# Optimization experiments

Hardware: AMD Instinct MI355X
Metric: run time of the kernel (lower is better)

Reference implementation:

```python
import jax, jax.numpy as jnp
import numpy as np

N_NODES = 256  # num_eeg_channels; reshape in head forces node count == channels

def setup_inputs() -> dict:
    key = jax.random.key(0)
    ks = jax.random.split(key, 16)
    T, H, L, E = 30000, 512, 256, 32768
    def w(k, shape):
        return jax.random.normal(k, shape, jnp.float32) / np.sqrt(shape[0]).astype(np.float32)
    return {
        "eeg_nodes": jax.random.normal(ks[0], (N_NODES, T), jnp.float32),
        "eeg_idx": jax.random.randint(ks[1], (2, E), 0, N_NODES),
        "eeg_attr": jax.random.uniform(ks[2], (E,), jnp.float32),
        # struct_featurizer GIN: conv1 MLP [T,H,H], conv2 MLP [H,L,L]
        "Ws1a": w(ks[3], (T, H)), "bs1a": jnp.zeros((H,), jnp.float32),
        "Ws1b": w(ks[4], (H, H)), "bs1b": jnp.zeros((H,), jnp.float32),
        "Ws2a": w(ks[5], (H, L)), "bs2a": jnp.zeros((L,), jnp.float32),
        "Ws2b": w(ks[6], (L, L)), "bs2b": jnp.zeros((L,), jnp.float32),
        # gin_scorer GIN: conv1 MLP [L,H,H], conv2 MLP [H,1,1]
        "Wc1a": w(ks[7], (L, H)), "bc1a": jnp.zeros((H,), jnp.float32),
        "Wc1b": w(ks[8], (H, H)), "bc1b": jnp.zeros((H,), jnp.float32),
        "Wc2a": w(ks[9], (H, 1)), "bc2a": jnp.zeros((1,), jnp.float32),
        "Wc2b": w(ks[10], (1, 1)), "bc2b": jnp.zeros((1,), jnp.float32),
        # dementia head: Linear(N*L, 1)
        "Wd": w(ks[11], (N_NODES * L, 1)), "bd": jnp.zeros((1,), jnp.float32),
    }


def _gin_conv(x, src, dst, W1, b1, W2, b2):
    # GINConv, eps=0: nn(x + sum_{j in N(i)} x_j); edge weights unsupported/ignored.
    agg = jax.ops.segment_sum(x[src], dst, num_segments=N_NODES)
    h = x + agg
    h = jax.nn.relu(h @ W1 + b1)  # MLP([in, out, out]) = Linear-ReLU-Linear
    return h @ W2 + b2


def reference(eeg_nodes, eeg_idx, eeg_attr,
              Ws1a, bs1a, Ws1b, bs1b, Ws2a, bs2a, Ws2b, bs2b,
              Wc1a, bc1a, Wc1b, bc1b, Wc2a, bc2a, Wc2b, bc2b,
              Wd, bd):
    src, dst = eeg_idx[0], eeg_idx[1]
    # struct_featurizer (2-layer GIN; inter-layer ReLU, edge_weight ignored by GINConv)
    h = _gin_conv(eeg_nodes, src, dst, Ws1a, bs1a, Ws1b, bs1b)
    h = jax.nn.relu(h)
    feat = _gin_conv(h, src, dst, Ws2a, bs2a, Ws2b, bs2b)  # [N, L]
    # gin_scorer (2-layer GIN)
    s = _gin_conv(feat, src, dst, Wc1a, bc1a, Wc1b, bc1b)
    s = jax.nn.relu(s)
    s = _gin_conv(s, src, dst, Wc2a, bc2a, Wc2b, bc2b)  # [N, 1]
    region_scores = jax.nn.sigmoid(s)
    flat = feat.reshape(1, -1)  # [1, N*L]
    dementia_pred = jax.nn.sigmoid(flat @ Wd + bd)  # [1, 1]
    return dementia_pred, region_scores
```

## Files before the change

kernel.cpp:

```cpp
#include <hip/hip_runtime.h>
#include <math.h>

#define N_NODES 256
#define T_DIM   30000
#define KP      30016
#define H_DIM   512
#define L_DIM   256

typedef __attribute__((ext_vector_type(8))) short short8;
typedef __attribute__((ext_vector_type(4))) float floatx4;

__global__ void k_init_P(float* P, float* dem, float* u) {
    int t = blockIdx.x * blockDim.x + threadIdx.x;
    P[t] = ((t >> 8) == (t & 255)) ? 1.0f : 0.0f;
    if (t == 0) *dem = 0.0f;
    if (t < 256) u[t] = 0.0f;
}

__global__ void k_count_edges(const int* __restrict__ idx, int E, float* P) {
    int e = blockIdx.x * blockDim.x + threadIdx.x;
    if (e < E) {
        int s = idx[e];
        int d = idx[E + e];
        atomicAdd(&P[d * N_NODES + s], 1.0f);
    }
}

__global__ void k_zero(float* p, int n) {
    int t = blockIdx.x * blockDim.x + threadIdx.x;
    if (t < n) p[t] = 0.0f;
}

__device__ __forceinline__ unsigned short f2b(float f) {
    unsigned u = __float_as_uint(f);
    u += 0x7fffu + ((u >> 16) & 1u);
    return (unsigned short)(u >> 16);
}

__device__ __forceinline__ float4 zero4() {
    float4 z; z.x = z.y = z.z = z.w = 0.f; return z;
}

__global__ __launch_bounds__(256)
void k_wt(const float* __restrict__ W, unsigned short* __restrict__ Wt) {
    __shared__ float tile[64][65];
    const int k0 = blockIdx.x << 6;
    const int c0 = blockIdx.y << 6;
    const int t  = threadIdx.x;
    const int rr = t >> 4, c4 = (t & 15) << 2;
    #pragma unroll
    for (int i = 0; i < 4; ++i) {
        const int k = k0 + rr + (i << 4);
        float4 v = (k < T_DIM) ? *(const float4*)&W[(size_t)k * H_DIM + c0 + c4]
                               : zero4();
        tile[rr + (i << 4)][c4 + 0] = v.x;
        tile[rr + (i << 4)][c4 + 1] = v.y;
        tile[rr + (i << 4)][c4 + 2] = v.z;
        tile[rr + (i << 4)][c4 + 3] = v.w;
    }
    __syncthreads();
    const int cr = t >> 4, k4 = (t & 15) << 2;
    #pragma unroll
    for (int i = 0; i < 4; ++i) {
        const int c = cr + (i << 4);
        ushort4 o;
        o.x = f2b(tile[k4 + 0][c]);
        o.y = f2b(tile[k4 + 1][c]);
        o.z = f2b(tile[k4 + 2][c]);
        o.w = f2b(tile[k4 + 3][c]);
        *(ushort4*)&Wt[(size_t)(c0 + c) * KP + k0 + k4] = o;
    }
}

__global__ __launch_bounds__(256)
void k_gemm_bf16(const float* __restrict__ x, const unsigned short* __restrict__ Wt,
                 float* __restrict__ outp, int kc) {
    __shared__ __align__(16) unsigned short Al[128 * 64];
    __shared__ __align__(16) unsigned short Bl[128 * 64];

    const int t = threadIdx.x;
    const int orig = blockIdx.x;
    const int q = gridDim.x >> 3;
    const int L = (orig & 7) * q + (orig >> 3);
    const int tile = L & 7;
    const int colBase = (tile & 3) << 7;
    const int rowBase = (tile >> 2) << 7;
    const int z = L >> 3;
    const int kb0 = z * kc;
    const int kend = min(kb0 + kc, KP);
    const int nchunk = (kend - kb0) >> 6;

    const int ar  = t >> 4, afc = t & 15;
    const int br  = t >> 3, bhc = t & 7;
    const float*          axp = x  + (size_t)(rowBase + ar) * T_DIM + afc * 4;
    const unsigned short* bwp = Wt + (size_t)(colBase + br) * KP   + bhc * 8;

    const int w    = t >> 6;
    const int wr   = (w >> 1) << 6;
    const int wc   = (w & 1) << 6;
    const int lane = t & 63;
    const int lm   = lane & 15;
    const int lq   = (lane >> 4) << 3;

    floatx4 acc[4][4];
    #pragma unroll
    for (int i = 0; i < 4; ++i)
        #pragma unroll
        for (int j = 0; j < 4; ++j)
            acc[i][j] = (floatx4){0.f, 0.f, 0.f, 0.f};

    float4 pa[8];
    short8 pb[4];

#define GLOAD(C) do {                                                          \
        const int kg_ = kb0 + (C) * 64;                                        \
        const int ke_ = kg_ + afc * 4;                                         \
        _Pragma("unroll")                                                      \
        for (int i_ = 0; i_ < 8; ++i_)                                         \
            pa[i_] = (ke_ + 4 <= T_DIM)                                        \
                         ? *(const float4*)(axp + (size_t)(16 * i_) * T_DIM + kg_) \
                         : zero4();                                            \
        _Pragma("unroll")                                                      \
        for (int i_ = 0; i_ < 4; ++i_)                                         \
            pb[i_] = *(const short8*)(bwp + (size_t)(32 * i_) * KP + kg_);     \
    } while (0)

    GLOAD(0);

    #pragma unroll 1
    for (int c = 0; c < nchunk; ++c) {
        __syncthreads();
        #pragma unroll
        for (int i = 0; i < 8; ++i) {
            const int row = ar + 16 * i;
            const int ga  = (afc >> 1) ^ (row & 7);
            ushort4 uv;
            uv.x = f2b(pa[i].x); uv.y = f2b(pa[i].y);
            uv.z = f2b(pa[i].z); uv.w = f2b(pa[i].w);
            *(ushort4*)&Al[row * 64 + ga * 8 + (afc & 1) * 4] = uv;
        }
        #pragma unroll
        for (int i = 0; i < 4; ++i) {
            const int row = br + 32 * i;
            const int gb  = bhc ^ (row & 7);
            *(short8*)&Bl[row * 64 + gb * 8] = pb[i];
        }
        __syncthreads();

        if (c + 1 < nchunk) GLOAD(c + 1);

        #pragma unroll
        for (int s = 0; s < 2; ++s) {
            const int gbase = (s << 2) | (lq >> 3);
            short8 af[4], bf[4];
            #pragma unroll
            for (int i = 0; i < 4; ++i) {
                const int R = wr + i * 16 + lm;
                af[i] = *(const short8*)&Al[R * 64 + ((gbase ^ (R & 7)) << 3)];
            }
            #pragma unroll
            for (int j = 0; j < 4; ++j) {
                const int Cc = wc + j * 16 + lm;
                bf[j] = *(const short8*)&Bl[Cc * 64 + ((gbase ^ (Cc & 7)) << 3)];
            }
            #pragma unroll
            for (int i = 0; i < 4; ++i)
                #pragma unroll
                for (int j = 0; j < 4; ++j)
                    acc[i][j] = __builtin_amdgcn_mfma_f32_16x16x32_bf16(
                        af[i], bf[j], acc[i][j], 0, 0, 0);
        }
    }
#undef GLOAD

    float* op = outp + (size_t)z * (N_NODES * H_DIM);
    const int rq = (lane >> 4) << 2;
    #pragma unroll
    for (int i = 0; i < 4; ++i) {
        #pragma unroll
        for (int j = 0; j < 4; ++j) {
            const int r  = rowBase + wr + i * 16 + rq;
            const int cc = colBase + wc + j * 16 + lm;
            op[(size_t)(r + 0) * H_DIM + cc] = acc[i][j][0];
            op[(size_t)(r + 1) * H_DIM + cc] = acc[i][j][1];
            op[(size_t)(r + 2) * H_DIM + cc] = acc[i][j][2];
            op[(size_t)(r + 3) * H_DIM + cc] = acc[i][j][3];
        }
    }
}

__global__ __launch_bounds__(256)
void k_gemm_big_atomic(const float* __restrict__ x, const float* __restrict__ W,
                       float* __restrict__ outp, int kc) {
    __shared__ float xs[16 * 140];
    __shared__ float ws[16 * 132];
    const int t  = threadIdx.x;
    const int colBase = blockIdx.x * 128;
    const int rowBase = blockIdx.y * 128;
    const int kb0  = blockIdx.z * kc;
    const int kend = min(kb0 + kc, T_DIM);
    const int nchunk = (kend > kb0) ? ((kend - kb0) >> 4) : 0;
    const int lr  = t >> 2, lkq = (t & 3) * 4;
    const int wkk = t >> 5, wcq = (t & 31) * 4;
    const int tx  = t & 15, ty = t >> 4;
    float acc[8][8];
    #pragma unroll
    for (int i = 0; i < 8; ++i)
        #pragma unroll
        for (int j = 0; j < 8; ++j) acc[i][j] = 0.0f;
    #pragma unroll 1
    for (int c = 0; c < nchunk; ++c) {
        int kb = kb0 + c * 16;
        __syncthreads();
        const float* xp = x + (size_t)(rowBase + lr) * T_DIM + kb + lkq;
        float4 xa = *(const float4*)xp;
        float4 xb = *(const float4*)(xp + (size_t)64 * T_DIM);
        const float* wp = W + (size_t)(kb + wkk) * H_DIM + colBase + wcq;
        float4 wa = *(const float4*)wp;
        float4 wb = *(const float4*)(wp + 8 * H_DIM);
        xs[(lkq + 0) * 140 + lr] = xa.x; xs[(lkq + 1) * 140 + lr] = xa.y;
        xs[(lkq + 2) * 140 + lr] = xa.z; xs[(lkq + 3) * 140 + lr] = xa.w;
        xs[(lkq + 0) * 140 + lr + 64] = xb.x; xs[(lkq + 1) * 140 + lr + 64] = xb.y;
        xs[(lkq + 2) * 140 + lr + 64] = xb.z; xs[(lkq + 3) * 140 + lr + 64] = xb.w;
        *(float4*)&ws[wkk * 132 + wcq]       = wa;
        *(float4*)&ws[(wkk + 8) * 132 + wcq] = wb;
        __syncthreads();
        #pragma unroll
        for (int kk = 0; kk < 16; ++kk) {
            float a[8], b[8];
            *(float4*)&a[0] = *(const float4*)&xs[kk * 140 + ty * 8];
            *(float4*)&a[4] = *(const float4*)&xs[kk * 140 + ty * 8 + 4];
            *(float4*)&b[0] = *(const float4*)&ws[kk * 132 + tx * 8];
            *(float4*)&b[4] = *(const float4*)&ws[kk * 132 + tx * 8 + 4];
            #pragma unroll
            for (int i = 0; i < 8; ++i)
                #pragma unroll
                for (int j = 0; j < 8; ++j)
                    acc[i][j] = fmaf(a[i], b[j], acc[i][j]);
        }
    }
    if (nchunk == 0) return;
    #pragma unroll
    for (int i = 0; i < 8; ++i) {
        int r = rowBase + ty * 8 + i;
        #pragma unroll
        for (int j = 0; j < 8; ++j)
            atomicAdd(&outp[r * H_DIM + colBase + tx * 8 + j], acc[i][j]);
    }
}

__global__ void k_reduce(const float2* __restrict__ Y1p, float2* __restrict__ Y1,
                         int nz) {
    int i = blockIdx.x * blockDim.x + threadIdx.x;
    float2 s = Y1p[i];
    for (int z = 1; z < nz; ++z) {
        float2 v = Y1p[(size_t)z * 65536 + i];
        s.x += v.x; s.y += v.y;
    }
    Y1[i] = s;
}

template<int K, int N, int MODE>
__global__ __launch_bounds__(256)
void k_mstage(const float* __restrict__ A, const float* __restrict__ B,
              const float* __restrict__ bias, float* __restrict__ out, int act,
              const float* __restrict__ Wd, float* __restrict__ dem,
              const float* __restrict__ uW, float* __restrict__ u) {
    const int t = threadIdx.x;
    const int wv = (blockIdx.x << 2) | (t >> 6);
    const int nct = N >> 4;
    const int r0 = (wv / nct) << 4;
    const int c0 = (wv % nct) << 4;
    const int lane = t & 63;
    const int lm   = lane & 15;
    const int lq   = (lane >> 4) << 3;

    floatx4 accE = {0.f, 0.f, 0.f, 0.f};
    floatx4 accO = {0.f, 0.f, 0.f, 0.f};
    const float* ap = A + (size_t)(r0 + lm) * K + lq;
    const float* bp = B + (size_t)lq * N + c0 + lm;

    #pragma unroll 2
    for (int kb = 0; kb < K; kb += 64) {
        {
            float4 a0 = *(const float4*)(ap + kb);
            float4 a1 = *(const float4*)(ap + kb + 4);
            const float* bq = bp + (size_t)kb * N;
            float b0 = bq[0],           b1 = bq[(size_t)N];
            float b2 = bq[(size_t)2*N], b3 = bq[(size_t)3*N];
            float b4 = bq[(size_t)4*N], b5 = bq[(size_t)5*N];
            float b6 = bq[(size_t)6*N], b7 = bq[(size_t)7*N];
            short8 af, bf;
            af[0] = (short)f2b(a0.x); af[1] = (short)f2b(a0.y);
            af[2] = (short)f2b(a0.z); af[3] = (short)f2b(a0.w);
            af[4] = (short)f2b(a1.x); af[5] = (short)f2b(a1.y);
            af[6] = (short)f2b(a1.z); af[7] = (short)f2b(a1.w);
            bf[0] = (short)f2b(b0); bf[1] = (short)f2b(b1);
            bf[2] = (short)f2b(b2); bf[3] = (short)f2b(b3);
            bf[4] = (short)f2b(b4); bf[5] = (short)f2b(b5);
            bf[6] = (short)f2b(b6); bf[7] = (short)f2b(b7);
            accE = __builtin_amdgcn_mfma_f32_16x16x32_bf16(af, bf, accE, 0, 0, 0);
        }
        {
            const int k2 = kb + 32;
            float4 a0 = *(const float4*)(ap + k2);
            float4 a1 = *(const float4*)(ap + k2 + 4);
            const float* bq = bp + (size_t)k2 * N;
            float b0 = bq[0],           b1 = bq[(size_t)N];
            float b2 = bq[(size_t)2*N], b3 = bq[(size_t)3*N];
            float b4 = bq[(size_t)4*N], b5 = bq[(size_t)5*N];
            float b6 = bq[(size_t)6*N], b7 = bq[(size_t)7*N];
            short8 af, bf;
            af[0] = (short)f2b(a0.x); af[1] = (short)f2b(a0.y);
            af[2] = (short)f2b(a0.z); af[3] = (short)f2b(a0.w);
            af[4] = (short)f2b(a1.x); af[5] = (short)f2b(a1.y);
            af[6] = (short)f2b(a1.z); af[7] = (short)f2b(a1.w);
            bf[0] = (short)f2b(b0); bf[1] = (short)f2b(b1);
            bf[2] = (short)f2b(b2); bf[3] = (short)f2b(b3);
            bf[4] = (short)f2b(b4); bf[5] = (short)f2b(b5);
            bf[6] = (short)f2b(b6); bf[7] = (short)f2b(b7);
            accO = __builtin_amdgcn_mfma_f32_16x16x32_bf16(af, bf, accO, 0, 0, 0);
        }
    }

    const float bb = bias ? bias[c0 + lm] : 0.f;
    const int rq = (lane >> 4) << 2;
    float v[4];
    #pragma unroll
    for (int i = 0; i < 4; ++i) {
        v[i] = accE[i] + accO[i] + bb;
        if (act) v[i] = fmaxf(v[i], 0.f);
    }

    if (MODE == 2) {
        const float uw = uW[c0 + lm];
        #pragma unroll
        for (int i = 0; i < 4; ++i) {
            float p = v[i] * uw;
            #pragma unroll
            for (int off = 8; off; off >>= 1) p += __shfl_down(p, off, 16);
            if (lm == 0) atomicAdd(&u[r0 + rq + i], p);
        }
        return;
    }
    #pragma unroll
    for (int i = 0; i < 4; ++i)
        out[(size_t)(r0 + rq + i) * N + c0 + lm] = v[i];
    if (MODE == 1) {
        float p = 0.f;
        #pragma unroll
        for (int i = 0; i < 4; ++i)
            p += v[i] * Wd[(r0 + rq + i) * 256 + c0 + lm];
        #pragma unroll
        for (int off = 32; off; off >>= 1) p += __shfl_down(p, off, 64);
        if (lane == 0) atomicAdd(dem, p);
    }
}

__device__ __forceinline__ float sigmoidf(float x) {
    return 1.0f / (1.0f + expf(-x));
}

__global__ __launch_bounds__(256)
void k_final(const float* __restrict__ P, const float* __restrict__ u,
             const float* __restrict__ dem,
             const float* __restrict__ bc2a, const float* __restrict__ Wc2b,
             const float* __restrict__ bc2b, const float* __restrict__ bd,
             float* __restrict__ out) {
    __shared__ float red[4];
    const int b = blockIdx.x, t = threadIdx.x;
    float pv = P[b * 256 + t] * u[t];
    #pragma unroll
    for (int off = 32; off; off >>= 1) pv += __shfl_down(pv, off, 64);
    if ((t & 63) == 0) red[t >> 6] = pv;
    __syncthreads();
    if (t == 0) {
        float v = red[0] + red[1] + red[2] + red[3];
        float h2 = fmaxf(v + bc2a[0], 0.f);
        out[1 + b] = sigmoidf(h2 * Wc2b[0] + bc2b[0]);
        if (b == 0) out[0] = sigmoidf(*dem + bd[0]);
    }
}

extern "C" void kernel_launch(void* const* d_in, const int* in_sizes, int n_in,
                              void* d_out, int out_size, void* d_ws, size_t ws_size,
                              hipStream_t stream) {
    const float* x    = (const float*)d_in[0];
    const int*   idx  = (const int*)d_in[1];
    const float* Ws1a = (const float*)d_in[3];
    const float* bs1a = (const float*)d_in[4];
    const float* Ws1b = (const float*)d_in[5];
    const float* bs1b = (const float*)d_in[6];
    const float* Ws2a = (const float*)d_in[7];
    const float* bs2a = (const float*)d_in[8];
    const float* Ws2b = (const float*)d_in[9];
    const float* bs2b = (const float*)d_in[10];
    const float* Wc1a = (const float*)d_in[11];
    const float* bc1a = (const float*)d_in[12];
    const float* Wc1b = (const float*)d_in[13];
    const float* bc1b = (const float*)d_in[14];
    const float* Wc2a = (const float*)d_in[15];
    const float* bc2a = (const float*)d_in[16];
    const float* Wc2b = (const float*)d_in[17];
    const float* bc2b = (const float*)d_in[18];
    const float* Wd   = (const float*)d_in[19];
    const float* bd   = (const float*)d_in[20];
    float* out = (float*)d_out;
    const int E = in_sizes[1] / 2;

    float* w    = (float*)d_ws;
    float* P    = w;
    float* Y1   = P + 65536;
    float* bufA = Y1 + 131072;
    float* bufB = bufA + 131072;
    float* feat = bufB + 131072;
    float* u    = feat + 65536;
    float* dem  = u + 256;
    float* WtF  = dem + 64;
    const size_t WT_F = ((size_t)H_DIM * KP) / 2;
    float* Y1p  = WtF + WT_F;
    unsigned short* Wt = (unsigned short*)WtF;

    const long long fixed = (long long)(Y1p - w);
    const long long avail = (long long)(ws_size / 4) - fixed;
    int maxsplit = (avail > 0) ? (int)(avail / 131072) : 0;
    int nz = 0, kc = 0;
    const int CH64 = 469;
    if (maxsplit >= 2) {
        int splits = maxsplit < 56 ? maxsplit : 56;
        int cps = (CH64 + splits - 1) / splits;
        nz = (CH64 + cps - 1) / cps;
        kc = cps * 64;
    }

    k_init_P<<<256, 256, 0, stream>>>(P, dem, u);
    k_count_edges<<<(E + 255) / 256, 256, 0, stream>>>(idx, E, P);

    if (nz > 0) {
        k_wt<<<dim3(469, 8), 256, 0, stream>>>(Ws1a, Wt);
        k_gemm_bf16<<<8 * nz, 256, 0, stream>>>(x, Wt, Y1p, kc);
        k_reduce<<<256, 256, 0, stream>>>((const float2*)Y1p, (float2*)Y1, nz);
    } else {
        k_zero<<<512, 256, 0, stream>>>(Y1, N_NODES * H_DIM);
        k_gemm_big_atomic<<<dim3(4, 2, 63), 256, 0, stream>>>(x, Ws1a, Y1, 480);
    }

    k_mstage<256, 512, 0><<<128, 256, 0, stream>>>(P,    Y1,   bs1a, bufA, 1, 0, 0, 0, 0);
    k_mstage<512, 512, 0><<<128, 256, 0, stream>>>(bufA, Ws1b, bs1b, bufB, 1, 0, 0, 0, 0);
    k_mstage<256, 512, 0><<<128, 256, 0, stream>>>(P,    bufB, 0,    bufA, 0, 0, 0, 0, 0);
    k_mstage<512, 256, 0><<< 64, 256, 0, stream>>>(bufA, Ws2a, bs2a, bufB, 1, 0, 0, 0, 0);
    k_mstage<256, 256, 1><<< 64, 256, 0, stream>>>(bufB, Ws2b, bs2b, feat, 0, Wd, dem, 0, 0);
    k_mstage<256, 256, 0><<< 64, 256, 0, stream>>>(P,    feat, 0,    bufA, 0, 0, 0, 0, 0);
    k_mstage<256, 512, 0><<<128, 256, 0, stream>>>(bufA, Wc1a, bc1a, bufB, 1, 0, 0, 0, 0);
    k_mstage<512, 512, 2><<<128, 256, 0, stream>>>(bufB, Wc1b, bc1b, 0,    1, 0, 0, Wc2a, u);
    k_final<<<256, 256, 0, stream>>>(P, u, dem, bc2a, Wc2b, bc2b, bd, out);
}
```

Baseline: 260.8 us.

## Pre-convert x to bf16 in a fused prep kernel and reshape small-GEMM launches

A single k_prep launch now does the W transpose to bf16, converts x to a padded bf16 copy, and initialises P, dem and u. Folding these into one kernel cuts launch count, and the big GEMM then loads bf16 activations directly instead of converting fp32 on each tile. The max split-K count rises from 56 to 96, and the reduce kernel uses float4 accesses. The k_mstage kernels switch to one wave per block with 4x more blocks, which spreads work over more CUs. The cost is an extra full pass writing x as bf16 plus more partial sums for the reduce to sum.

```diff
diff --git a/kernel.cpp b/kernel.cpp
--- a/kernel.cpp
+++ b/kernel.cpp
@@ -10,11 +10,78 @@
 typedef __attribute__((ext_vector_type(8))) short short8;
 typedef __attribute__((ext_vector_type(4))) float floatx4;
 
-__global__ void k_init_P(float* P, float* dem, float* u) {
-    int t = blockIdx.x * blockDim.x + threadIdx.x;
-    P[t] = ((t >> 8) == (t & 255)) ? 1.0f : 0.0f;
-    if (t == 0) *dem = 0.0f;
-    if (t < 256) u[t] = 0.0f;
+__device__ __forceinline__ unsigned short f2b(float f) {
+    unsigned u = __float_as_uint(f);
+    u += 0x7fffu + ((u >> 16) & 1u);
+    return (unsigned short)(u >> 16);
+}
+
+__device__ __forceinline__ float4 zero4() {
+    float4 z; z.x = z.y = z.z = z.w = 0.f; return z;
+}
+
+__global__ __launch_bounds__(256)
+void k_prep(const float* __restrict__ W, const float* __restrict__ x,
+            unsigned short* __restrict__ Wt, unsigned short* __restrict__ xb,
+            float* __restrict__ P, float* __restrict__ dem,
+            float* __restrict__ u) {
+    __shared__ float tile[64][65];
+    const int b = blockIdx.x, t = threadIdx.x;
+    if (b < 3752) {
+        const int k0 = (b % 469) << 6;
+        const int c0 = (b / 469) << 6;
+        const int rr = t >> 4, c4 = (t & 15) << 2;
+        #pragma unroll
+        for (int i = 0; i < 4; ++i) {
+            const int k = k0 + rr + (i << 4);
+            float4 v = (k < T_DIM)
+                           ? *(const float4*)&W[(size_t)k * H_DIM + c0 + c4]
+                           : zero4();
+            tile[rr + (i << 4)][c4 + 0] = v.x;
+            tile[rr + (i << 4)][c4 + 1] = v.y;
+            tile[rr + (i << 4)][c4 + 2] = v.z;
+            tile[rr + (i << 4)][c4 + 3] = v.w;
+        }
+        __syncthreads();
+        const int cr = t >> 4, k4 = (t & 15) << 2;
+        #pragma unroll
+        for (int i = 0; i < 4; ++i) {
+            const int c = cr + (i << 4);
+            ushort4 o;
+            o.x = f2b(tile[k4 + 0][c]);
+            o.y = f2b(tile[k4 + 1][c]);
+            o.z = f2b(tile[k4 + 2][c]);
+            o.w = f2b(tile[k4 + 3][c]);
+            *(ushort4*)&Wt[(size_t)(c0 + c) * KP + k0 + k4] = o;
+        }
+    } else if (b < 7504) {
+        const int e0 = (b - 3752) * 2048 + t * 8;
+        const int row = e0 / KP;
+        const int col = e0 % KP;
+        short8 o;
+        if (col < T_DIM) {
+            float4 v0 = *(const float4*)&x[(size_t)row * T_DIM + col];
+            float4 v1 = *(const float4*)&x[(size_t)row * T_DIM + col + 4];
+            o[0] = (short)f2b(v0.x); o[1] = (short)f2b(v0.y);
+            o[2] = (short)f2b(v0.z); o[3] = (short)f2b(v0.w);
+            o[4] = (short)f2b(v1.x); o[5] = (short)f2b(v1.y);
+            o[6] = (short)f2b(v1.z); o[7] = (short)f2b(v1.w);
+        } else {
+            o = (short8){0, 0, 0, 0, 0, 0, 0, 0};
+        }
+        *(short8*)&xb[e0] = o;
+    } else if (b < 7568) {
+        const int i0 = ((b - 7504) << 10) + (t << 2);
+        float4 v;
+        v.x = ((i0 + 0) >> 8) == ((i0 + 0) & 255) ? 1.f : 0.f;
+        v.y = ((i0 + 1) >> 8) == ((i0 + 1) & 255) ? 1.f : 0.f;
+        v.z = ((i0 + 2) >> 8) == ((i0 + 2) & 255) ? 1.f : 0.f;
+        v.w = ((i0 + 3) >> 8) == ((i0 + 3) & 255) ? 1.f : 0.f;
+        *(float4*)&P[i0] = v;
+    } else {
+        if (t < 256) u[t] = 0.f;
+        if (t == 0) *dem = 0.f;
+    }
 }
 
 __global__ void k_count_edges(const int* __restrict__ idx, int E, float* P) {
@@ -26,54 +93,21 @@
     }
 }
 
+__global__ void k_init_P(float* P, float* dem, float* u) {
+    int t = blockIdx.x * blockDim.x + threadIdx.x;
+    P[t] = ((t >> 8) == (t & 255)) ? 1.0f : 0.0f;
+    if (t == 0) *dem = 0.0f;
+    if (t < 256) u[t] = 0.0f;
+}
+
 __global__ void k_zero(float* p, int n) {
     int t = blockIdx.x * blockDim.x + threadIdx.x;
     if (t < n) p[t] = 0.0f;
 }
 
-__device__ __forceinline__ unsigned short f2b(float f) {
-    unsigned u = __float_as_uint(f);
-    u += 0x7fffu + ((u >> 16) & 1u);
-    return (unsigned short)(u >> 16);
-}
-
-__device__ __forceinline__ float4 zero4() {
-    float4 z; z.x = z.y = z.z = z.w = 0.f; return z;
-}
-
 __global__ __launch_bounds__(256)
-void k_wt(const float* __restrict__ W, unsigned short* __restrict__ Wt) {
-    __shared__ float tile[64][65];
-    const int k0 = blockIdx.x << 6;
-    const int c0 = blockIdx.y << 6;
-    const int t  = threadIdx.x;
-    const int rr = t >> 4, c4 = (t & 15) << 2;
-    #pragma unroll
-    for (int i = 0; i < 4; ++i) {
-        const int k = k0 + rr + (i << 4);
-        float4 v = (k < T_DIM) ? *(const float4*)&W[(size_t)k * H_DIM + c0 + c4]
-                               : zero4();
-        tile[rr + (i << 4)][c4 + 0] = v.x;
-        tile[rr + (i << 4)][c4 + 1] = v.y;
-        tile[rr + (i << 4)][c4 + 2] = v.z;
-        tile[rr + (i << 4)][c4 + 3] = v.w;
-    }
-    __syncthreads();
-    const int cr = t >> 4, k4 = (t & 15) << 2;
-    #pragma unroll
-    for (int i = 0; i < 4; ++i) {
-        const int c = cr + (i << 4);
-        ushort4 o;
-        o.x = f2b(tile[k4 + 0][c]);
-        o.y = f2b(tile[k4 + 1][c]);
-        o.z = f2b(tile[k4 + 2][c]);
-        o.w = f2b(tile[k4 + 3][c]);
-        *(ushort4*)&Wt[(size_t)(c0 + c) * KP + k0 + k4] = o;
-    }
-}
-
-__global__ __launch_bounds__(256)
-void k_gemm_bf16(const float* __restrict__ x, const unsigned short* __restrict__ Wt,
+void k_gemm_bf16(const unsigned short* __restrict__ xb,
+                 const unsigned short* __restrict__ Wt,
                  float* __restrict__ outp, int kc) {
     __shared__ __align__(16) unsigned short Al[128 * 64];
     __shared__ __align__(16) unsigned short Bl[128 * 64];
@@ -90,10 +124,10 @@
     const int kend = min(kb0 + kc, KP);
     const int nchunk = (kend - kb0) >> 6;
 
-    const int ar  = t >> 4, afc = t & 15;
-    const int br  = t >> 3, bhc = t & 7;
-    const float*          axp = x  + (size_t)(rowBase + ar) * T_DIM + afc * 4;
-    const unsigned short* bwp = Wt + (size_t)(colBase + br) * KP   + bhc * 8;
+    const int sr = t >> 1, sg = (t & 1) << 2;
+    const int br = t >> 3, bhc = t & 7;
+    const unsigned short* axp = xb + (size_t)(rowBase + sr) * KP + sg * 8;
+    const unsigned short* bwp = Wt + (size_t)(colBase + br) * KP + bhc * 8;
 
     const int w    = t >> 6;
     const int wr   = (w >> 1) << 6;
@@ -109,17 +143,13 @@
         for (int j = 0; j < 4; ++j)
             acc[i][j] = (floatx4){0.f, 0.f, 0.f, 0.f};
 
-    float4 pa[8];
-    short8 pb[4];
+    short8 pa[4], pb[4];
 
 #define GLOAD(C) do {                                                          \
         const int kg_ = kb0 + (C) * 64;                                        \
-        const int ke_ = kg_ + afc * 4;                                         \
         _Pragma("unroll")                                                      \
-        for (int i_ = 0; i_ < 8; ++i_)                                         \
-            pa[i_] = (ke_ + 4 <= T_DIM)                                        \
-                         ? *(const float4*)(axp + (size_t)(16 * i_) * T_DIM + kg_) \
-                         : zero4();                                            \
+        for (int i_ = 0; i_ < 4; ++i_)                                         \
+            pa[i_] = *(const short8*)(axp + kg_ + i_ * 8);                     \
         _Pragma("unroll")                                                      \
         for (int i_ = 0; i_ < 4; ++i_)                                         \
             pb[i_] = *(const short8*)(bwp + (size_t)(32 * i_) * KP + kg_);     \
@@ -131,13 +161,9 @@
     for (int c = 0; c < nchunk; ++c) {
         __syncthreads();
         #pragma unroll
-        for (int i = 0; i < 8; ++i) {
-            const int row = ar + 16 * i;
-            const int ga  = (afc >> 1) ^ (row & 7);
-            ushort4 uv;
-            uv.x = f2b(pa[i].x); uv.y = f2b(pa[i].y);
-            uv.z = f2b(pa[i].z); uv.w = f2b(pa[i].w);
-            *(ushort4*)&Al[row * 64 + ga * 8 + (afc & 1) * 4] = uv;
+        for (int i = 0; i < 4; ++i) {
+            const int ga = (sg + i) ^ (sr & 7);
+            *(short8*)&Al[sr * 64 + ga * 8] = pa[i];
         }
         #pragma unroll
         for (int i = 0; i < 4; ++i) {
@@ -214,14 +240,14 @@
         __syncthreads();
         const float* xp = x + (size_t)(rowBase + lr) * T_DIM + kb + lkq;
         float4 xa = *(const float4*)xp;
-        float4 xb = *(const float4*)(xp + (size_t)64 * T_DIM);
+        float4 xb4 = *(const float4*)(xp + (size_t)64 * T_DIM);
         const float* wp = W + (size_t)(kb + wkk) * H_DIM + colBase + wcq;
         float4 wa = *(const float4*)wp;
         float4 wb = *(const float4*)(wp + 8 * H_DIM);
         xs[(lkq + 0) * 140 + lr] = xa.x; xs[(lkq + 1) * 140 + lr] = xa.y;
         xs[(lkq + 2) * 140 + lr] = xa.z; xs[(lkq + 3) * 140 + lr] = xa.w;
-        xs[(lkq + 0) * 140 + lr + 64] = xb.x; xs[(lkq + 1) * 140 + lr + 64] = xb.y;
-        xs[(lkq + 2) * 140 + lr + 64] = xb.z; xs[(lkq + 3) * 140 + lr + 64] = xb.w;
+        xs[(lkq + 0) * 140 + lr + 64] = xb4.x; xs[(lkq + 1) * 140 + lr + 64] = xb4.y;
+        xs[(lkq + 2) * 140 + lr + 64] = xb4.z; xs[(lkq + 3) * 140 + lr + 64] = xb4.w;
         *(float4*)&ws[wkk * 132 + wcq]       = wa;
         *(float4*)&ws[(wkk + 8) * 132 + wcq] = wb;
         __syncthreads();
@@ -249,29 +275,28 @@
     }
 }
 
-__global__ void k_reduce(const float2* __restrict__ Y1p, float2* __restrict__ Y1,
+__global__ void k_reduce(const float4* __restrict__ Y1p, float4* __restrict__ Y1,
                          int nz) {
     int i = blockIdx.x * blockDim.x + threadIdx.x;
-    float2 s = Y1p[i];
+    float4 s = Y1p[i];
     for (int z = 1; z < nz; ++z) {
-        float2 v = Y1p[(size_t)z * 65536 + i];
-        s.x += v.x; s.y += v.y;
+        float4 v = Y1p[(size_t)z * 32768 + i];
+        s.x += v.x; s.y += v.y; s.z += v.z; s.w += v.w;
     }
     Y1[i] = s;
 }
 
 template<int K, int N, int MODE>
-__global__ __launch_bounds__(256)
+__global__ __launch_bounds__(64)
 void k_mstage(const float* __restrict__ A, const float* __restrict__ B,
               const float* __restrict__ bias, float* __restrict__ out, int act,
               const float* __restrict__ Wd, float* __restrict__ dem,
               const float* __restrict__ uW, float* __restrict__ u) {
-    const int t = threadIdx.x;
-    const int wv = (blockIdx.x << 2) | (t >> 6);
+    const int lane = threadIdx.x;
+    const int wv = blockIdx.x;
     const int nct = N >> 4;
     const int r0 = (wv / nct) << 4;
     const int c0 = (wv % nct) << 4;
-    const int lane = t & 63;
     const int lm   = lane & 15;
     const int lq   = (lane >> 4) << 3;
 
@@ -418,8 +443,11 @@
     float* dem  = u + 256;
     float* WtF  = dem + 64;
     const size_t WT_F = ((size_t)H_DIM * KP) / 2;
-    float* Y1p  = WtF + WT_F;
+    float* XbF  = WtF + WT_F;
+    const size_t XB_F = ((size_t)N_NODES * KP) / 2;
+    float* Y1p  = XbF + XB_F;
     unsigned short* Wt = (unsigned short*)WtF;
+    unsigned short* xb = (unsigned short*)XbF;
 
     const long long fixed = (long long)(Y1p - w);
     const long long avail = (long long)(ws_size / 4) - fixed;
@@ -427,31 +455,31 @@
     int nz = 0, kc = 0;
     const int CH64 = 469;
     if (maxsplit >= 2) {
-        int splits = maxsplit < 56 ? maxsplit : 56;
+        int splits = maxsplit < 96 ? maxsplit : 96;
         int cps = (CH64 + splits - 1) / splits;
         nz = (CH64 + cps - 1) / cps;
         kc = cps * 64;
     }
 
-    k_init_P<<<256, 256, 0, stream>>>(P, dem, u);
-    k_count_edges<<<(E + 255) / 256, 256, 0, stream>>>(idx, E, P);
-
     if (nz > 0) {
-        k_wt<<<dim3(469, 8), 256, 0, stream>>>(Ws1a, Wt);
-        k_gemm_bf16<<<8 * nz, 256, 0, stream>>>(x, Wt, Y1p, kc);
-        k_reduce<<<256, 256, 0, stream>>>((const float2*)Y1p, (float2*)Y1, nz);
+        k_prep<<<7569, 256, 0, stream>>>(Ws1a, x, Wt, xb, P, dem, u);
+        k_count_edges<<<(E + 255) / 256, 256, 0, stream>>>(idx, E, P);
+        k_gemm_bf16<<<8 * nz, 256, 0, stream>>>(xb, Wt, Y1p, kc);
+        k_reduce<<<128, 256, 0, stream>>>((const float4*)Y1p, (float4*)Y1, nz);
     } else {
+        k_init_P<<<256, 256, 0, stream>>>(P, dem, u);
+        k_count_edges<<<(E + 255) / 256, 256, 0, stream>>>(idx, E, P);
         k_zero<<<512, 256, 0, stream>>>(Y1, N_NODES * H_DIM);
         k_gemm_big_atomic<<<dim3(4, 2, 63), 256, 0, stream>>>(x, Ws1a, Y1, 480);
     }
 
-    k_mstage<256, 512, 0><<<128, 256, 0, stream>>>(P,    Y1,   bs1a, bufA, 1, 0, 0, 0, 0);
-    k_mstage<512, 512, 0><<<128, 256, 0, stream>>>(bufA, Ws1b, bs1b, bufB, 1, 0, 0, 0, 0);
-    k_mstage<256, 512, 0><<<128, 256, 0, stream>>>(P,    bufB, 0,    bufA, 0, 0, 0, 0, 0);
-    k_mstage<512, 256, 0><<< 64, 256, 0, stream>>>(bufA, Ws2a, bs2a, bufB, 1, 0, 0, 0, 0);
-    k_mstage<256, 256, 1><<< 64, 256, 0, stream>>>(bufB, Ws2b, bs2b, feat, 0, Wd, dem, 0, 0);
-    k_mstage<256, 256, 0><<< 64, 256, 0, stream>>>(P,    feat, 0,    bufA, 0, 0, 0, 0, 0);
-    k_mstage<256, 512, 0><<<128, 256, 0, stream>>>(bufA, Wc1a, bc1a, bufB, 1, 0, 0, 0, 0);
-    k_mstage<512, 512, 2><<<128, 256, 0, stream>>>(bufB, Wc1b, bc1b, 0,    1, 0, 0, Wc2a, u);
+    k_mstage<256, 512, 0><<<512, 64, 0, stream>>>(P,    Y1,   bs1a, bufA, 1, 0, 0, 0, 0);
+    k_mstage<512, 512, 0><<<512, 64, 0, stream>>>(bufA, Ws1b, bs1b, bufB, 1, 0, 0, 0, 0);
+    k_mstage<256, 512, 0><<<512, 64, 0, stream>>>(P,    bufB, 0,    bufA, 0, 0, 0, 0, 0);
+    k_mstage<512, 256, 0><<<256, 64, 0, stream>>>(bufA, Ws2a, bs2a, bufB, 1, 0, 0, 0, 0);
+    k_mstage<256, 256, 1><<<256, 64, 0, stream>>>(bufB, Ws2b, bs2b, feat, 0, Wd, dem, 0, 0);
+    k_mstage<256, 256, 0><<<256, 64, 0, stream>>>(P,    feat, 0,    bufA, 0, 0, 0, 0, 0);
+    k_mstage<256, 512, 0><<<512, 64, 0, stream>>>(bufA, Wc1a, bc1a, bufB, 1, 0, 0, 0, 0);
+    k_mstage<512, 512, 2><<<512, 64, 0, stream>>>(bufB, Wc1b, bc1b, 0,    1, 0, 0, Wc2a, u);
     k_final<<<256, 256, 0, stream>>>(P, u, dem, bc2a, Wc2b, bc2b, bd, out);
 }
```

Result: faster. 247.3 us (-5.2%).
